# Performance work log

Measured on AMD Instinct MI355X. Metric: run time of the kernel, lower is better.

## Reference

```python
import jax, jax.numpy as jnp
import numpy as np

NL, NS, NE = 16, 256, 100   # nlatent, nspatial, n_embd
B, P, T = 2, 2, 12


def _xavier(key, shape):
    # torch xavier_uniform: fan_in = shape[1]*prod(rest), fan_out = shape[0]*prod(rest)
    rf = int(np.prod(shape[2:])) if len(shape) > 2 else 1
    fan_in, fan_out = shape[1] * rf, shape[0] * rf
    b = float(np.sqrt(6.0 / (fan_in + fan_out)))
    return jax.random.uniform(key, shape, jnp.float32, -b, b)


def setup_inputs() -> dict:
    key = jax.random.key(0)
    ks = jax.random.split(key, 8)
    x = jax.random.normal(ks[0], (B, P, T, NL, NS), jnp.float32)
    K = _xavier(ks[1], (NS, NS, NL))
    Q = _xavier(ks[2], (NS, NS, NL))
    V = _xavier(ks[3], (NS, NS, NL))
    Aoo = jnp.ones((NS, NS), jnp.float32)
    # Ann is initialized to zeros in the module; use nonzero values so the
    # clamped geometric recurrence over time is actually exercised.
    Ann = jax.random.uniform(ks[4], (NE,), jnp.float32, -0.9, 0.9)
    Aon = _xavier(ks[5], (NS, NS, NE))
    Ano = _xavier(ks[6], (NS, NS, NE))
    w = jnp.ones((NS,), jnp.float32) / NS
    return {"x": x, "K": K, "Q": Q, "V": V, "Aoo": Aoo,
            "Ann": Ann, "Aon": Aon, "Ano": Ano, "w": w}


def reference(x, K, Q, V, Aoo, Ann, Aon, Ano, w):
    # kvt[B,p,T,X,Y] = sum_{x,c} Q[Y,x,c] K[X,x,c] x[B,p,T,c,x]
    kvt = jnp.einsum('Yxc,Xxc,BpTcx->BpTXY', Q, K, x)
    Aon_c = jnp.clip(Aon, -1.0, 1.0)
    Ano_c = jnp.clip(Ano, -1.0, 1.0)

    # t = T-1 term (elementwise Aoo) and t = T-2 term
    h = Aoo[None, None, None] * kvt[:, :, -1:]
    h = h + jnp.einsum('xyn,XYn,BpTXY->BpTxy', Aon_c, Ano_c, kvt[:, :, -2:-1])

    nT = x.shape[2]
    # Ann sequence used in the loop: A_2 = Ann (raw), A_{j+1} = clip(A_j * Ann)
    def step(a, _):
        return jnp.clip(a * Ann, -1.0, 1.0), a
    _, A_seq = jax.lax.scan(step, Ann, None, length=nT - 2)  # [T-2, n], A_seq[j-2]=A_j

    # loop index j=2..T-1 touches time slice t = T-1-j, i.e. t = T-3 .. 0
    s = jnp.einsum('XYn,BpJXY->BpJn', Ano_c, kvt[:, :, :nT - 2])  # J = t in 0..T-3
    A_t = A_seq[::-1]                       # align A_j with time index t = T-1-j
    s2 = jnp.einsum('Jn,BpJn->Bpn', A_t, s)
    h = h + jnp.einsum('xyn,Bpn->Bpxy', Aon_c, s2)[:, :, None]  # [B,p,1,x,y]

    q = jnp.einsum('Xxc,Bpcx->BpcX', V, x[:, :, -1])
    y = jnp.einsum('x,BpcX,BpTXx->BpTc', w, q, h)  # [B,p,1,c]
    return y
```

## Files before the change

kernel.cpp:

```cpp
#include <hip/hip_runtime.h>
#include <hip/hip_fp16.h>


using f32x4 = __attribute__((ext_vector_type(4))) float;
using half8 = __attribute__((ext_vector_type(8))) _Float16;
using half4 = __attribute__((ext_vector_type(4))) _Float16;

#define KVT_STRIDE 3145728ull
#define KS 4

__device__ inline float clip1(float v) { return fminf(fmaxf(v, -1.f), 1.f); }

__device__ inline half8 mul8(uint4 a, uint4 b) {
    half8 x = __builtin_bit_cast(half8, a);
    half8 y = __builtin_bit_cast(half8, b);
    return x * y;
}

__device__ __forceinline__ void gl_lds16(const void* g, void* l) {
    __builtin_amdgcn_global_load_lds(
        (const __attribute__((address_space(1))) void*)g,
        (__attribute__((address_space(3))) void*)l, 16, 0, 0);
}

__global__ void prep_kernel(const float* __restrict__ K, const float* __restrict__ Q,
                            const float* __restrict__ xin,
                            const float* __restrict__ Aon, const float* __restrict__ wv,
                            const float* __restrict__ V,
                            __half* __restrict__ Kh, __half* __restrict__ Qh,
                            __half* __restrict__ u_t,
                            float* __restrict__ W2p, float* __restrict__ R)
{
    int b = blockIdx.x, t = threadIdx.x;
    if (b < 2048) {
        bool isK = (b < 1024);
        int bb = isK ? b : b - 1024;
        int i = bb * 1024 + t * 4;
        const float4 f = ((const float4*)(isK ? K : Q))[i >> 2];
        half4 v = { (_Float16)f.x, (_Float16)f.y, (_Float16)f.z, (_Float16)f.w };
        *(half4*)((isK ? Kh : Qh) + i) = v;
    } else if (b < 2096) {
        int bt = b - 2048;
        const float* src = xin + (size_t)bt * 4096;
        int xx = t;
        half8 lo, hi;
        #pragma unroll
        for (int c = 0; c < 8; ++c)  lo[c] = (_Float16)src[c * 256 + xx];
        #pragma unroll
        for (int c = 0; c < 8; ++c)  hi[c] = (_Float16)src[(c + 8) * 256 + xx];
        half8* dst = (half8*)(u_t + (size_t)bt * 4096 + xx * 16);
        dst[0] = lo; dst[1] = hi;
    } else if (b < 2608) {
        int idx = b - 2096;
        int X = idx >> 1, h = idx & 1;
        int g = h * 2 + (t >> 7), n = t & 127;
        if (n < 100) {
            const float* base = Aon + (size_t)X * 25600 + (size_t)g * 6400 + n;
            float acc = 0.f;
            for (int bb = 0; bb < 64; ++bb)
                acc += wv[g * 64 + bb] * clip1(__builtin_nontemporal_load(base + (size_t)bb * 100));
            W2p[((size_t)g * 256 + X) * 100 + n] = acc;
        }
    } else {
        __shared__ float vrow[4096];
        int X = b - 2608;
        {
            const float4* src = (const float4*)(V + (size_t)X * 4096);
            float4* dst = (float4*)vrow;
            for (int i = t; i < 1024; i += 256) dst[i] = src[i];
        }
        __syncthreads();
        int bp = t >> 6, c = (t >> 2) & 15, g = t & 3;
        const float* xl = xin + ((size_t)(bp * 12) + 11) * 4096 + c * 256;
        float p = 0.f;
        #pragma unroll 4
        for (int x = g * 64; x < g * 64 + 64; ++x)
            p += xl[x] * vrow[x * 16 + c];
        p += __shfl_xor(p, 1);
        p += __shfl_xor(p, 2);
        if (g == 0) R[((size_t)bp * 256 + X) * 16 + c] = p;
    }
}

__global__ __launch_bounds__(256, 4) void gemm_kvt(
    const __half* __restrict__ Kh, const __half* __restrict__ Qh,
    const __half* __restrict__ u_t, __half* __restrict__ kvtp)
{
    __shared__ __half As[2][128][32];
    __shared__ __half Bs[2][128][32];
    __shared__ __half u_s[1024];

    int bid = blockIdx.x;
    int work = (bid & 7) * 96 + (bid >> 3);
    int kc = work / 192;
    int rem = work - kc * 192;
    int tile = rem / 48;
    int bt = rem - tile * 48;
    int Xb = (tile >> 1) * 128, Yb = (tile & 1) * 128;
    int kbase = kc * 1024;

    int tid = threadIdx.x;
    if (tid < 128)
        *(uint4*)&u_s[tid * 8] = *(const uint4*)(u_t + (size_t)bt * 4096 + kbase + tid * 8);
    __syncthreads();

    int wave = tid >> 6, lane = tid & 63;
    int srow = lane >> 2;
    int sk = ((lane & 3) ^ ((srow >> 1) & 3)) << 3;
    const __half* gA = Kh + (size_t)(Xb + wave * 16 + srow) * 4096 + kbase + sk;
    const __half* gB = Qh + (size_t)(Yb + wave * 16 + srow) * 4096 + kbase + sk;

    int wr = (wave >> 1) * 64, wc = (wave & 1) * 64;
    int lrow = lane & 15, kg = lane >> 4;
    int fb = (kg * 16) ^ (((lrow >> 1) & 3) << 4);

    f32x4 acc[4][4];
    f32x4 zero = {0.f, 0.f, 0.f, 0.f};
    #pragma unroll
    for (int m = 0; m < 4; ++m)
        #pragma unroll
        for (int n = 0; n < 4; ++n) acc[m][n] = zero;

    #define STAGE(s, buf)                                                      \
        do {                                                                   \
            _Pragma("unroll")                                                  \
            for (int i_ = 0; i_ < 2; ++i_) {                                   \
                gl_lds16(gA + (size_t)(i_ * 64) * 4096 + (s) * 32,             \
                         &As[buf][i_ * 64 + wave * 16][0]);                    \
                gl_lds16(gB + (size_t)(i_ * 64) * 4096 + (s) * 32,             \
                         &Bs[buf][i_ * 64 + wave * 16][0]);                    \
            }                                                                  \
        } while (0)

    STAGE(0, 0);
    STAGE(1, 1);

    for (int s = 0; s < 32; ++s) {
        if (s < 31) asm volatile("s_waitcnt vmcnt(4)" ::: "memory");
        else        asm volatile("s_waitcnt vmcnt(0)" ::: "memory");
        __builtin_amdgcn_s_barrier();
        __builtin_amdgcn_sched_barrier(0);

        int cur = s & 1;
        uint4 uv = *(const uint4*)&u_s[s * 32 + kg * 8];
        half8 af[4], bf[4];
        #pragma unroll
        for (int m = 0; m < 4; ++m)
            af[m] = mul8(*(const uint4*)((const char*)&As[cur][wr + m * 16 + lrow][0] + fb), uv);
        #pragma unroll
        for (int n = 0; n < 4; ++n)
            bf[n] = *(const half8*)((const char*)&Bs[cur][wc + n * 16 + lrow][0] + fb);
        #pragma unroll
        for (int m = 0; m < 4; ++m)
            #pragma unroll
            for (int n = 0; n < 4; ++n)
                acc[m][n] = __builtin_amdgcn_mfma_f32_16x16x32_f16(af[m], bf[n], acc[m][n], 0, 0, 0);

        asm volatile("s_waitcnt lgkmcnt(0)" ::: "memory");
        __builtin_amdgcn_s_barrier();
        __builtin_amdgcn_sched_barrier(0);
        if (s + 2 < 32) STAGE(s + 2, cur);
    }
    #undef STAGE

    __half* outp = kvtp + (size_t)kc * KVT_STRIDE + (size_t)bt * 65536;
    int row0 = Xb + wr + kg * 4;
    int col0 = Yb + wc + lrow;
    #pragma unroll
    for (int m = 0; m < 4; ++m)
        #pragma unroll
        for (int n = 0; n < 4; ++n)
            #pragma unroll
            for (int rr = 0; rr < 4; ++rr)
                outp[(size_t)(row0 + m * 16 + rr) * 256 + col0 + n * 16] =
                    __float2half(acc[m][n][rr]);
}

__global__ __launch_bounds__(256) void s_partial(const float* __restrict__ Ano,
                                                 const __half* __restrict__ kvtp,
                                                 float* __restrict__ Sp)
{
    __shared__ float ano_f[12864];
    __shared__ float kvt_s[44][128];
    int cb = blockIdx.x;
    int k0 = cb * 128;
    int tid = threadIdx.x;

    {
        const f32x4* src = (const f32x4*)(Ano + (size_t)k0 * 100);
        f32x4* dst = (f32x4*)ano_f;
        for (int i = tid; i < 3200; i += 256) {
            f32x4 f = __builtin_nontemporal_load(src + i);
            f.x = clip1(f.x); f.y = clip1(f.y); f.z = clip1(f.z); f.w = clip1(f.w);
            dst[i] = f;
        }
    }
    {
        for (int idx = tid; idx < 5632; idx += 256) {
            int rI = idx >> 7, k = idx & 127;
            int bpr = rI / 11, Jr = rI - bpr * 11;
            size_t off = (size_t)(bpr * 12 + Jr) * 65536 + k0 + k;
            float v = 0.f;
            #pragma unroll
            for (int c = 0; c < KS; ++c)
                v += __half2float(kvtp[(size_t)c * KVT_STRIDE + off]);
            kvt_s[rI][k] = v;
        }
    }
    __syncthreads();

    int lane = tid & 63;
    int bp = tid >> 6;
    bool has2 = lane < 36;
    float acc0[11], acc1[11];
    #pragma unroll
    for (int J = 0; J < 11; ++J) { acc0[J] = 0.f; acc1[J] = 0.f; }

    for (int k = 0; k < 128; k += 4) {
        f32x4 kv[11];
        #pragma unroll
        for (int J = 0; J < 11; ++J)
            kv[J] = *(const f32x4*)&kvt_s[bp * 11 + J][k];
        #pragma unroll
        for (int kk = 0; kk < 4; ++kk) {
            float a0 = ano_f[(k + kk) * 100 + lane];
            float a1r = ano_f[(k + kk) * 100 + 64 + lane];
            float a1 = has2 ? a1r : 0.f;
            #pragma unroll
            for (int J = 0; J < 11; ++J) {
                acc0[J] += kv[J][kk] * a0;
                acc1[J] += kv[J][kk] * a1;
            }
        }
    }
    float* outb = Sp + ((size_t)cb * 4 + bp) * 1100;
    #pragma unroll
    for (int J = 0; J < 11; ++J) {
        outb[J * 100 + lane] = acc0[J];
        if (has2) outb[J * 100 + 64 + lane] = acc1[J];
    }
}

__global__ void reduce_s(const float* __restrict__ Sp, float* __restrict__ Sq,
                         float* __restrict__ out)
{
    int bid = blockIdx.x;
    int t = threadIdx.x;
    if (bid == 0 && t < 64) out[t] = 0.f;
    int qq = bid & 3, idx = bid >> 2;
    int bp = idx / 11, J = idx - bp * 11;
    if (t >= 100) return;
    float acc = 0.f;
    for (int c = qq * 128; c < qq * 128 + 128; ++c)
        acc += Sp[((size_t)c * 4 + bp) * 1100 + J * 100 + t];
    Sq[(size_t)(qq * 44 + idx) * 100 + t] = acc;
}

__global__ __launch_bounds__(256) void hw_kernel(const float* __restrict__ Aoo,
                                                 const float* __restrict__ wv,
                                                 const __half* __restrict__ kvtp,
                                                 const float* __restrict__ W2p,
                                                 const float* __restrict__ Sq,
                                                 const float* __restrict__ Ann,
                                                 const float* __restrict__ R,
                                                 float* __restrict__ out)
{
    __shared__ float yp[4][16];
    __shared__ float c2s[128];
    int bp = blockIdx.x >> 6, Xg = blockIdx.x & 63;
    int tid = threadIdx.x;

    if (tid < 128) {
        int n = tid;
        float r = 0.f;
        if (n < 100) {
            float S[11];
            #pragma unroll
            for (int J = 0; J < 11; ++J) {
                float s = 0.f;
                #pragma unroll
                for (int qq = 0; qq < 4; ++qq)
                    s += Sq[(size_t)(qq * 44 + bp * 11 + J) * 100 + n];
                S[J] = s;
            }
            float a = Ann[n];
            float seq[10];
            float v = a;
            seq[0] = v;
            #pragma unroll
            for (int s2 = 1; s2 < 10; ++s2) { v = clip1(v * a); seq[s2] = v; }
            r = S[10];
            #pragma unroll
            for (int J = 0; J < 10; ++J)
                r += seq[9 - J] * S[J];
        }
        c2s[n] = r;
    }
    __syncthreads();

    int wave = tid >> 6, lane = tid & 63;
    int X = Xg * 4 + wave;
    size_t base = (size_t)(bp * 12 + 11) * 65536 + (size_t)X * 256;
    const float* ao = Aoo + (size_t)X * 256;
    float red = 0.f;
    #pragma unroll
    for (int qq = 0; qq < 4; ++qq) {
        int xx = qq * 64 + lane;
        float kvv = 0.f;
        #pragma unroll
        for (int c = 0; c < KS; ++c)
            kvv += __half2float(kvtp[(size_t)c * KVT_STRIDE + base + xx]);
        red += wv[xx] * ao[xx] * kvv;
    }
    float w2a = 0.f, w2b = 0.f;
    #pragma unroll
    for (int g = 0; g < 4; ++g) {
        w2a += W2p[((size_t)g * 256 + X) * 100 + lane];
        if (lane < 36) w2b += W2p[((size_t)g * 256 + X) * 100 + 64 + lane];
    }
    red += c2s[lane] * w2a;
    if (lane < 36)
        red += c2s[64 + lane] * w2b;
    #pragma unroll
    for (int off = 32; off; off >>= 1) red += __shfl_xor(red, off);
    if (lane < 16) yp[wave][lane] = red * R[((size_t)bp * 256 + X) * 16 + lane];
    __syncthreads();
    if (tid < 16) {
        float s = yp[0][tid] + yp[1][tid] + yp[2][tid] + yp[3][tid];
        atomicAdd(&out[bp * 16 + tid], s);
    }
}

extern "C" void kernel_launch(void* const* d_in, const int* in_sizes, int n_in,
                              void* d_out, int out_size, void* d_ws, size_t ws_size,
                              hipStream_t stream)
{
    const float* x   = (const float*)d_in[0];
    const float* K   = (const float*)d_in[1];
    const float* Q   = (const float*)d_in[2];
    const float* V   = (const float*)d_in[3];
    const float* Aoo = (const float*)d_in[4];
    const float* Ann = (const float*)d_in[5];
    const float* Aon = (const float*)d_in[6];
    const float* Ano = (const float*)d_in[7];
    const float* wv  = (const float*)d_in[8];
    float* out = (float*)d_out;

    char* ws = (char*)d_ws;
    const size_t o_Qh   = 0;
    const size_t o_Kh   = o_Qh + (size_t)2 * 1024 * 1024;
    const size_t o_ut   = o_Kh + (size_t)2 * 1024 * 1024;
    const size_t o_kvtp = o_ut + (size_t)512 * 1024;
    const size_t o_Sp   = o_kvtp + (size_t)KS * KVT_STRIDE * 2;
    const size_t o_Sq   = o_Sp + (size_t)512 * 4400 * 4;
    const size_t o_W2   = o_Sq + (size_t)17600 * 4 + 64;
    const size_t o_R    = o_W2 + (size_t)102400 * 4;

    __half* Qh  = (__half*)(ws + o_Qh);
    __half* Kh  = (__half*)(ws + o_Kh);
    __half* u_t = (__half*)(ws + o_ut);
    __half* kvtp = (__half*)(ws + o_kvtp);
    float* Sp   = (float*)(ws + o_Sp);
    float* Sq   = (float*)(ws + o_Sq);
    float* W2p  = (float*)(ws + o_W2);
    float* R    = (float*)(ws + o_R);

    hipLaunchKernelGGL(prep_kernel, dim3(2864), dim3(256), 0, stream,
                       K, Q, x, Aon, wv, V, Kh, Qh, u_t, W2p, R);
    hipLaunchKernelGGL(gemm_kvt,    dim3(768),  dim3(256), 0, stream, Kh, Qh, u_t, kvtp);
    hipLaunchKernelGGL(s_partial,   dim3(512),  dim3(256), 0, stream, Ano, kvtp, Sp);
    hipLaunchKernelGGL(reduce_s,    dim3(176),  dim3(128), 0, stream, Sp, Sq, out);
    hipLaunchKernelGGL(hw_kernel,   dim3(256),  dim3(256), 0, stream,
                       Aoo, wv, kvtp, W2p, Sq, Ann, R, out);
}
```

Measured before the change: 105.1 us.

## Prescale K tile by u once via register staging instead of per-fragment multiply

The K operand tile now comes through registers instead of the direct global-to-LDS path. It is multiplied by the u vector once when written to LDS, rather than each wave multiplying its A fragments by u every k-step. This removes redundant half multiplies from the MFMA inner loop. The cost is extra VGPRs and explicit LDS stores for A, and the global loads of A become a register-prefetch pipeline interleaved with the B direct loads. The vmcnt accounting now mixes register loads with LDS loads, which risks stalls or ordering subtlety.

New measurement: 104.2 us. Within noise of the previous version (-0.8%).

```diff
diff --git a/kernel.cpp b/kernel.cpp
--- a/kernel.cpp
+++ b/kernel.cpp
@@ -105,9 +105,16 @@
     __syncthreads();
 
     int wave = tid >> 6, lane = tid & 63;
+
+    int arow = tid >> 1;
+    int apair = (tid & 1) * 2;
+    const __half* gA = Kh + (size_t)(Xb + arow) * 4096 + kbase + apair * 8;
+    int aswz = (arow >> 1) & 3;
+    int asb0 = ((apair + 0) ^ aswz) << 4;
+    int asb1 = ((apair + 1) ^ aswz) << 4;
+
     int srow = lane >> 2;
     int sk = ((lane & 3) ^ ((srow >> 1) & 3)) << 3;
-    const __half* gA = Kh + (size_t)(Xb + wave * 16 + srow) * 4096 + kbase + sk;
     const __half* gB = Qh + (size_t)(Yb + wave * 16 + srow) * 4096 + kbase + sk;
 
     int wr = (wave >> 1) * 64, wc = (wave & 1) * 64;
@@ -121,47 +128,75 @@
         #pragma unroll
         for (int n = 0; n < 4; ++n) acc[m][n] = zero;
 
-    #define STAGE(s, buf)                                                      \
+    #define ISSUE_B(s, buf)                                                    \
         do {                                                                   \
             _Pragma("unroll")                                                  \
-            for (int i_ = 0; i_ < 2; ++i_) {                                   \
-                gl_lds16(gA + (size_t)(i_ * 64) * 4096 + (s) * 32,             \
-                         &As[buf][i_ * 64 + wave * 16][0]);                    \
+            for (int i_ = 0; i_ < 2; ++i_)                                     \
                 gl_lds16(gB + (size_t)(i_ * 64) * 4096 + (s) * 32,             \
                          &Bs[buf][i_ * 64 + wave * 16][0]);                    \
+        } while (0)
+
+    #define WRITE_A(s, r0, r1, buf)                                            \
+        do {                                                                   \
+            uint4 uv0 = *(const uint4*)&u_s[(s) * 32 + apair * 8];             \
+            uint4 uv1 = *(const uint4*)&u_s[(s) * 32 + apair * 8 + 8];         \
+            *(half8*)((char*)&As[buf][arow][0] + asb0) = mul8(r0, uv0);        \
+            *(half8*)((char*)&As[buf][arow][0] + asb1) = mul8(r1, uv1);        \
+        } while (0)
+
+    #define COMPUTE(cur)                                                       \
+        do {                                                                   \
+            half8 af[4], bf[4];                                                \
+            _Pragma("unroll")                                                  \
+            for (int m = 0; m < 4; ++m)                                        \
+                af[m] = *(const half8*)((const char*)&As[cur][wr + m * 16 + lrow][0] + fb); \
+            _Pragma("unroll")                                                  \
+            for (int n = 0; n < 4; ++n)                                        \
+                bf[n] = *(const half8*)((const char*)&Bs[cur][wc + n * 16 + lrow][0] + fb); \
+            _Pragma("unroll")                                                  \
+            for (int m = 0; m < 4; ++m)                                        \
+                _Pragma("unroll")                                              \
+                for (int n = 0; n < 4; ++n)                                    \
+                    acc[m][n] = __builtin_amdgcn_mfma_f32_16x16x32_f16(af[m], bf[n], acc[m][n], 0, 0, 0); \
+        } while (0)
+
+    #define STEP(s, c0, c1, i0, i1, cur)                                       \
+        do {                                                                   \
+            if ((s) < 31) asm volatile("s_waitcnt vmcnt(4) lgkmcnt(0)" ::: "memory"); \
+            else          asm volatile("s_waitcnt vmcnt(0) lgkmcnt(0)" ::: "memory"); \
+            __builtin_amdgcn_s_barrier();                                      \
+            __builtin_amdgcn_sched_barrier(0);                                 \
+            COMPUTE(cur);                                                      \
+            asm volatile("s_waitcnt lgkmcnt(0)" ::: "memory");                 \
+            __builtin_amdgcn_s_barrier();                                      \
+            __builtin_amdgcn_sched_barrier(0);                                 \
+            if ((s) + 2 < 32) {                                                \
+                const __half* a_ = gA + ((s) + 2) * 32;                        \
+                i0 = *(const uint4*)a_;                                        \
+                i1 = *(const uint4*)(a_ + 8);                                  \
+                ISSUE_B((s) + 2, cur);                                         \
             }                                                                  \
+            if ((s) + 1 < 32) WRITE_A((s) + 1, c0, c1, (cur) ^ 1);             \
         } while (0)
 
-    STAGE(0, 0);
-    STAGE(1, 1);
-
-    for (int s = 0; s < 32; ++s) {
-        if (s < 31) asm volatile("s_waitcnt vmcnt(4)" ::: "memory");
-        else        asm volatile("s_waitcnt vmcnt(0)" ::: "memory");
-        __builtin_amdgcn_s_barrier();
-        __builtin_amdgcn_sched_barrier(0);
-
-        int cur = s & 1;
-        uint4 uv = *(const uint4*)&u_s[s * 32 + kg * 8];
-        half8 af[4], bf[4];
-        #pragma unroll
-        for (int m = 0; m < 4; ++m)
-            af[m] = mul8(*(const uint4*)((const char*)&As[cur][wr + m * 16 + lrow][0] + fb), uv);
-        #pragma unroll
-        for (int n = 0; n < 4; ++n)
-            bf[n] = *(const half8*)((const char*)&Bs[cur][wc + n * 16 + lrow][0] + fb);
-        #pragma unroll
-        for (int m = 0; m < 4; ++m)
-            #pragma unroll
-            for (int n = 0; n < 4; ++n)
-                acc[m][n] = __builtin_amdgcn_mfma_f32_16x16x32_f16(af[m], bf[n], acc[m][n], 0, 0, 0);
-
-        asm volatile("s_waitcnt lgkmcnt(0)" ::: "memory");
-        __builtin_amdgcn_s_barrier();
-        __builtin_amdgcn_sched_barrier(0);
-        if (s + 2 < 32) STAGE(s + 2, cur);
-    }
-    #undef STAGE
+    uint4 aP0, aP1, aC0, aC1;
+    aP0 = *(const uint4*)gA;
+    aP1 = *(const uint4*)(gA + 8);
+    ISSUE_B(0, 0);
+    aC0 = *(const uint4*)(gA + 32);
+    aC1 = *(const uint4*)(gA + 40);
+    ISSUE_B(1, 1);
+    WRITE_A(0, aP0, aP1, 0);
+
+    #pragma unroll
+    for (int s = 0; s < 32; s += 2) {
+        STEP(s,     aC0, aC1, aP0, aP1, 0);
+        STEP(s + 1, aP0, aP1, aC0, aC1, 1);
+    }
+    #undef STEP
+    #undef COMPUTE
+    #undef WRITE_A
+    #undef ISSUE_B
 
     __half* outp = kvtp + (size_t)kc * KVT_STRIDE + (size_t)bt * 65536;
     int row0 = Xb + wr + kg * 4;
```
